# Optimization experiments

Measured on AMD Instinct MI355X. Metric: run time of the kernel, lower is better.

The kernel has to match this reference:

```python
import jax, jax.numpy as jnp
import numpy as np

DIM, D_STATE, D_CONV, EXPAND = 1024, 16, 4, 2
D_INNER = EXPAND * DIM
DT_RANK = (DIM + 15) // 16  # 64
B, L = 2, 1024


def setup_inputs() -> dict:
    key = jax.random.key(0)
    ks = jax.random.split(key, 12)
    s = lambda k, shp, sc: jax.random.normal(k, shp, jnp.float32) * sc
    return {
        "x": s(ks[0], (B, L, DIM), 1.0),
        "ln_g": jnp.ones((DIM,), jnp.float32),
        "ln_b": jnp.zeros((DIM,), jnp.float32),
        "W_in": s(ks[1], (DIM, 2 * D_INNER), DIM ** -0.5),
        "conv_w": s(ks[2], (D_INNER, D_CONV), D_CONV ** -0.5),
        "conv_b": jnp.zeros((D_INNER,), jnp.float32),
        "W_x": s(ks[3], (D_INNER, DT_RANK + 2 * D_STATE), D_INNER ** -0.5),
        "W_dt": s(ks[4], (DT_RANK, D_INNER), DT_RANK ** -0.5),
        "b_dt": s(ks[5], (D_INNER,), 0.1),
        "A_log": jnp.log(jnp.broadcast_to(jnp.arange(1, D_STATE + 1, dtype=jnp.float32), (D_INNER, D_STATE))),
        "D_skip": jnp.ones((D_INNER,), jnp.float32),
        "W_out": s(ks[6], (D_INNER, DIM), D_INNER ** -0.5),
    }


def _mamba_block(x, ln_g, ln_b, W_in, conv_w, conv_b, W_x, W_dt, b_dt, A_log, D_skip, W_out):
    # LayerNorm over feature dim
    mu = jnp.mean(x, -1, keepdims=True)
    var = jnp.mean(jnp.square(x - mu), -1, keepdims=True)
    xn = (x - mu) * jax.lax.rsqrt(var + 1e-5) * ln_g + ln_b

    # in_proj -> (u, z), each (B, L, E)
    u, z = jnp.split(xn @ W_in, 2, axis=-1)

    # causal depthwise conv1d over L (kernel D_CONV) + SiLU
    up = jnp.pad(u, ((0, 0), (D_CONV - 1, 0), (0, 0)))
    uc = conv_b
    for k in range(D_CONV):
        uc = uc + conv_w[:, k] * up[:, k:k + L, :]
    uc = jax.nn.silu(uc)

    # input-dependent dt, B, C
    dbl = uc @ W_x
    dt = jax.nn.softplus(dbl[..., :DT_RANK] @ W_dt + b_dt)      # (B,L,E)
    Bc = dbl[..., DT_RANK:DT_RANK + D_STATE]                    # (B,L,N)
    Cc = dbl[..., DT_RANK + D_STATE:]                           # (B,L,N)

    A = -jnp.exp(A_log)                                         # (E,N)
    dA = jnp.exp(dt[..., None] * A)                             # (B,L,E,N)
    dBu = (dt * uc)[..., None] * Bc[:, :, None, :]              # (B,L,E,N)

    # selective scan: h_t = dA_t * h_{t-1} + dBu_t  (associative)
    def comb(c1, c2):
        a1, b1 = c1
        a2, b2 = c2
        return a2 * a1, a2 * b1 + b2

    _, h = jax.lax.associative_scan(comb, (dA, dBu), axis=1)

    y = jnp.einsum('blen,bln->ble', h, Cc) + uc * D_skip
    y = y * jax.nn.silu(z)
    return y @ W_out                                            # (B,L,DIM)


def reference(x, ln_g, ln_b, W_in, conv_w, conv_b, W_x, W_dt, b_dt, A_log, D_skip, W_out):
    return _mamba_block(x, ln_g, ln_b, W_in, conv_w, conv_b, W_x, W_dt, b_dt, A_log, D_skip, W_out)
```

## Files before the change

### kernel.cpp

```cpp
#include <hip/hip_runtime.h>
#include <hip/hip_bf16.h>

typedef __attribute__((ext_vector_type(4))) float  f32x4;
typedef __attribute__((ext_vector_type(8))) __bf16 bf16x8;

typedef __attribute__((address_space(1))) void gvoid_t;
typedef __attribute__((address_space(3))) void lvoid_t;

__device__ __forceinline__ void gld16(const void* g, void* l) {
    __builtin_amdgcn_global_load_lds((const gvoid_t*)g, (lvoid_t*)l, 16, 0, 0);
}

template <int N> __device__ __forceinline__ void vwait() {
    if constexpr (N == 0)      asm volatile("s_waitcnt vmcnt(0)" ::: "memory");
    else if constexpr (N == 6) asm volatile("s_waitcnt vmcnt(6)" ::: "memory");
    else if constexpr (N == 8) asm volatile("s_waitcnt vmcnt(8)" ::: "memory");
}

__device__ __forceinline__ unsigned short f2bf(float f) {
    unsigned u = __builtin_bit_cast(unsigned, f);
    u += 0x7fffu + ((u >> 16) & 1u);
    return (unsigned short)(u >> 16);
}
__device__ __forceinline__ float bf2f(unsigned short u) {
    return __builtin_bit_cast(float, (unsigned)u << 16);
}
__device__ __forceinline__ float silu(float x) {
    return x / (1.f + __expf(-x));
}

__device__ __forceinline__ void tr_cvt(const float* __restrict__ in,
                                       unsigned short* __restrict__ out,
                                       int K, int N, int Npad, int bnb, int bkb,
                                       float* sh) {
    float (*t)[33] = (float(*)[33])sh;
    int bn = bnb * 32, bk = bkb * 32;
    int c = threadIdx.x & 31, r0 = threadIdx.x >> 5;
    #pragma unroll
    for (int rr = r0; rr < 32; rr += 8) {
        int k = bk + rr, n = bn + c;
        t[rr][c] = (k < K && n < N) ? in[(size_t)k * N + n] : 0.f;
    }
    __syncthreads();
    #pragma unroll
    for (int rr = r0; rr < 32; rr += 8) {
        int n = bn + rr, k = bk + c;
        if (n < Npad && k < K) out[(size_t)n * K + k] = f2bf(t[c][rr]);
    }
}

__global__ __launch_bounds__(256) void k_prep(const float* __restrict__ x,
                                              const float* __restrict__ g,
                                              const float* __restrict__ b,
                                              unsigned short* __restrict__ xn,
                                              const float* __restrict__ W_in,  unsigned short* __restrict__ WIN_T,
                                              const float* __restrict__ W_out, unsigned short* __restrict__ WOUT_T,
                                              const float* __restrict__ W_dt,  unsigned short* __restrict__ WDT_T,
                                              const float* __restrict__ W_x,   unsigned short* __restrict__ WX_T) {
    __shared__ float sh[32 * 33];
    int bid = blockIdx.x;
    if (bid < 2048) {
        int row = bid;
        const float4* xr = (const float4*)(x + (size_t)row * 1024);
        float4 v = xr[threadIdx.x];
        float s  = v.x + v.y + v.z + v.w;
        float ss = v.x*v.x + v.y*v.y + v.z*v.z + v.w*v.w;
        #pragma unroll
        for (int o = 32; o > 0; o >>= 1) { s += __shfl_down(s, o); ss += __shfl_down(ss, o); }
        if ((threadIdx.x & 63) == 0) { sh[threadIdx.x >> 6] = s; sh[4 + (threadIdx.x >> 6)] = ss; }
        __syncthreads();
        s  = sh[0] + sh[1] + sh[2] + sh[3];
        ss = sh[4] + sh[5] + sh[6] + sh[7];
        float mu  = s * (1.f / 1024.f);
        float inv = rsqrtf(ss * (1.f / 1024.f) - mu * mu + 1e-5f);
        float4 gv = ((const float4*)g)[threadIdx.x];
        float4 bv = ((const float4*)b)[threadIdx.x];
        ushort4 o4;
        o4.x = f2bf((v.x - mu) * inv * gv.x + bv.x);
        o4.y = f2bf((v.y - mu) * inv * gv.y + bv.y);
        o4.z = f2bf((v.z - mu) * inv * gv.z + bv.z);
        o4.w = f2bf((v.w - mu) * inv * gv.w + bv.w);
        ((ushort4*)xn)[(size_t)row * 256 + threadIdx.x] = o4;
    } else if (bid < 6144) {
        int i = bid - 2048;  tr_cvt(W_in,  WIN_T,  1024, 4096, 4096, i & 127, i >> 7, sh);
    } else if (bid < 8192) {
        int i = bid - 6144;  tr_cvt(W_out, WOUT_T, 2048, 1024, 1024, i & 31,  i >> 5, sh);
    } else if (bid < 8320) {
        int i = bid - 8192;  tr_cvt(W_dt,  WDT_T,  64,   2048, 2048, i & 63,  i >> 6, sh);
    } else {
        int i = bid - 8320;  tr_cvt(W_x,   WX_T,   2048, 96,   128,  i & 3,   i >> 2, sh);
    }
}

template <int BM, int BN, int EPI>
__global__ __launch_bounds__(256) void k_gemm2(const unsigned short* __restrict__ A,
                                               const unsigned short* __restrict__ Bt,
                                               float* __restrict__ C,
                                               unsigned short* __restrict__ C2,
                                               unsigned short* __restrict__ C3,
                                               int kchunk, int lda, int ldb, int ldc,
                                               size_t zstride,
                                               const float* __restrict__ bias) {
    constexpr int PA = BM / 32, PB = BN / 32, NV = PA + PB;
    constexpr int MF = BM / 32, NF = BN / 32;
    __shared__ __attribute__((aligned(16))) unsigned short smA[2 * BM * 64];
    __shared__ __attribute__((aligned(16))) unsigned short smB[2 * BN * 64];

    int tid = threadIdx.x, wave = tid >> 6, lane = tid & 63;
    int bm = blockIdx.x * BM, bn = blockIdx.y * BN;
    int kstart = blockIdx.z * kchunk;
    int nt = kchunk >> 6;
    C += (size_t)blockIdx.z * zstride;
    int wm = (wave >> 1) * (BM / 2), wn = (wave & 1) * (BN / 2);
    int lr = lane & 15, lq = lane >> 4;
    int srow = wave * 8 + (lane >> 3);
    int scg  = lane & 7;

    f32x4 acc[MF][NF] = {};

    auto STAGE = [&](int buf, int k0) {
        unsigned short* dA = smA + buf * (BM * 64) + wave * 512;
        unsigned short* dB = smB + buf * (BN * 64) + wave * 512;
        #pragma unroll
        for (int p = 0; p < PA; ++p) {
            int row = p * 32 + srow;
            int gcol = ((scg ^ (row & 7)) << 3) + k0;
            gld16(A + (size_t)(bm + row) * lda + gcol, dA + p * 2048);
        }
        #pragma unroll
        for (int p = 0; p < PB; ++p) {
            int row = p * 32 + srow;
            int gcol = ((scg ^ (row & 7)) << 3) + k0;
            gld16(Bt + (size_t)(bn + row) * ldb + gcol, dB + p * 2048);
        }
    };

    STAGE(0, kstart);
    for (int t = 0; t < nt; ++t) {
        int cur = t & 1;
        if (t + 1 < nt) { STAGE(cur ^ 1, kstart + (t + 1) * 64); vwait<NV>(); }
        else            { vwait<0>(); }
        __builtin_amdgcn_s_barrier();
        const unsigned short* sA = smA + cur * (BM * 64);
        const unsigned short* sB = smB + cur * (BN * 64);
        #pragma unroll
        for (int ks = 0; ks < 2; ++ks) {
            int cg = (ks * 4 + lq) ^ (lr & 7);
            bf16x8 af[MF], bfv[NF];
            #pragma unroll
            for (int i = 0; i < MF; ++i)
                af[i] = *(const bf16x8*)(sA + (wm + i * 16 + lr) * 64 + (cg << 3));
            #pragma unroll
            for (int i = 0; i < NF; ++i)
                bfv[i] = *(const bf16x8*)(sB + (wn + i * 16 + lr) * 64 + (cg << 3));
            #pragma unroll
            for (int mi = 0; mi < MF; ++mi)
                #pragma unroll
                for (int ni = 0; ni < NF; ++ni)
                    acc[mi][ni] = __builtin_amdgcn_mfma_f32_16x16x32_bf16(af[mi], bfv[ni], acc[mi][ni], 0, 0, 0);
        }
        __builtin_amdgcn_s_barrier();
    }

    #pragma unroll
    for (int mi = 0; mi < MF; ++mi) {
        #pragma unroll
        for (int ni = 0; ni < NF; ++ni) {
            int c = bn + wn + ni * 16 + lr;
            #pragma unroll
            for (int v = 0; v < 4; ++v) {
                int r = bm + wm + mi * 16 + (lq << 2) + v;
                float val = acc[mi][ni][v];
                if (EPI == 0) {
                    C[(size_t)r * ldc + c] = val;
                } else if (EPI == 1) {
                    val += bias[c];
                    val = (val > 20.f) ? val : log1pf(__expf(val));
                    C[(size_t)r * ldc + c] = val;
                } else {
                    if (c < 2048) C2[(size_t)r * 2048 + c] = f2bf(val);
                    else          C3[(size_t)r * 2048 + (c - 2048)] = f2bf(silu(val));
                }
            }
        }
    }
}

__global__ __launch_bounds__(256) void k_red8(const float* __restrict__ part,
                                              float* __restrict__ dbl,
                                              unsigned short* __restrict__ dtr) {
    int idx = blockIdx.x * 256 + threadIdx.x;
    float s = 0.f;
    #pragma unroll
    for (int z = 0; z < 8; ++z) s += part[(size_t)z * 262144 + idx];
    dbl[idx] = s;
    int r = idx >> 7, c = idx & 127;
    if (c < 64) dtr[r * 64 + c] = f2bf(s);
}

__global__ __launch_bounds__(256) void k_conv2(const unsigned short* __restrict__ UB,
                                               const float* __restrict__ cw,
                                               const float* __restrict__ cb,
                                               unsigned short* __restrict__ ucb) {
    int idx = blockIdx.x * 256 + threadIdx.x;
    int e  = idx & 2047;
    int bl = idx >> 11;
    int l  = bl & 1023;
    float acc = cb[e];
    float4 wv = *(const float4*)(cw + e * 4);
    float w4[4] = {wv.x, wv.y, wv.z, wv.w};
    #pragma unroll
    for (int k = 0; k < 4; ++k) {
        int ls = l - 3 + k;
        if (ls >= 0) acc += w4[k] * bf2f(UB[(size_t)(bl - 3 + k) * 2048 + e]);
    }
    ucb[idx] = f2bf(silu(acc));
}


__global__ __launch_bounds__(256) void k_scan_p1(const unsigned short* __restrict__ ucb,
                                                 const float* __restrict__ dt,
                                                 const float* __restrict__ dbl,
                                                 const float* __restrict__ A_log,
                                                 float* __restrict__ aggH,
                                                 float* __restrict__ sdtb) {
    __shared__ float sB[32][16];
    int bid = blockIdx.x;
    int c = bid & 31, eblk = (bid >> 5) & 7, b = bid >> 8;
    int t = threadIdx.x;
    int e = eblk * 256 + t;
    int bl0 = b * 1024 + c * 32;
    if (t < 128) {
        int r = t >> 2, j4 = t & 3;
        *(float4*)&sB[r][j4 * 4] = *(const float4*)(dbl + (size_t)(bl0 + r) * 128 + 64 + j4 * 4);
    }
    __syncthreads();
    float Aen[16];
    #pragma unroll
    for (int n = 0; n < 16; ++n) Aen[n] = -__expf(A_log[e * 16 + n]);
    bool fastA = true;
    #pragma unroll
    for (int n = 1; n < 16; ++n)
        fastA = fastA && (fabsf(Aen[n] - (n + 1) * Aen[0]) <= 1e-3f);
    float h[16];
    #pragma unroll
    for (int n = 0; n < 16; ++n) h[n] = 0.f;
    float sdt = 0.f;
    size_t iu = (size_t)bl0 * 2048 + e;
    #pragma unroll 4
    for (int l = 0; l < 32; ++l) {
        float dtv = dt[iu];
        float ucv = bf2f(ucb[iu]);
        float dtu = dtv * ucv;
        float dA[16];
        if (fastA) {
            float p = __expf(dtv * Aen[0]);
            float cur = p;
            #pragma unroll
            for (int n = 0; n < 16; ++n) { dA[n] = cur; cur *= p; }
        } else {
            #pragma unroll
            for (int n = 0; n < 16; ++n) dA[n] = __expf(dtv * Aen[n]);
        }
        #pragma unroll
        for (int n = 0; n < 16; ++n)
            h[n] = fmaf(dA[n], h[n], dtu * sB[l][n]);
        sdt += dtv;
        iu += 2048;
    }
    size_t o = ((size_t)(b * 32 + c) * 16) * 2048 + e;
    #pragma unroll
    for (int n = 0; n < 16; ++n) aggH[o + (size_t)n * 2048] = h[n];
    sdtb[(size_t)(b * 32 + c) * 2048 + e] = sdt;
}

__global__ __launch_bounds__(256) void k_scan_p3(const unsigned short* __restrict__ ucb,
                                                 const float* __restrict__ dt,
                                                 const float* __restrict__ dbl,
                                                 const unsigned short* __restrict__ sz,
                                                 const float* __restrict__ A_log,
                                                 const float* __restrict__ D_skip,
                                                 const float* __restrict__ aggH,
                                                 const float* __restrict__ sdtb,
                                                 unsigned short* __restrict__ yg) {
    __shared__ float sBC[32][32];
    int bid = blockIdx.x;
    int c = bid & 31, eblk = (bid >> 5) & 7, b = bid >> 8;
    int t = threadIdx.x;
    int e = eblk * 256 + t;
    int bl0 = b * 1024 + c * 32;
    {
        int r = t >> 3, j = t & 7;
        *(float4*)&sBC[r][j * 4] = *(const float4*)(dbl + (size_t)(bl0 + r) * 128 + 64 + j * 4);
    }
    __syncthreads();
    float Aen[16];
    #pragma unroll
    for (int n = 0; n < 16; ++n) Aen[n] = -__expf(A_log[e * 16 + n]);
    bool fastA = true;
    #pragma unroll
    for (int n = 1; n < 16; ++n)
        fastA = fastA && (fabsf(Aen[n] - (n + 1) * Aen[0]) <= 1e-3f);
    float De = D_skip[e];
    float h[16];
    #pragma unroll
    for (int n = 0; n < 16; ++n) h[n] = 0.f;
    for (int cc = 0; cc < c; ++cc) {
        float sdtc = sdtb[(size_t)(b * 32 + cc) * 2048 + e];
        size_t oa = ((size_t)(b * 32 + cc) * 16) * 2048 + e;
        float aa[16];
        if (fastA) {
            float p = __expf(sdtc * Aen[0]);
            float cur = p;
            #pragma unroll
            for (int n = 0; n < 16; ++n) { aa[n] = cur; cur *= p; }
        } else {
            #pragma unroll
            for (int n = 0; n < 16; ++n) aa[n] = __expf(sdtc * Aen[n]);
        }
        #pragma unroll
        for (int n = 0; n < 16; ++n)
            h[n] = fmaf(aa[n], h[n], aggH[oa + (size_t)n * 2048]);
    }
    size_t iu = (size_t)bl0 * 2048 + e;
    #pragma unroll 4
    for (int l = 0; l < 32; ++l) {
        float dtv = dt[iu];
        float ucv = bf2f(ucb[iu]);
        float szv = bf2f(sz[iu]);
        float dtu = dtv * ucv;
        float dA[16];
        if (fastA) {
            float p = __expf(dtv * Aen[0]);
            float cur = p;
            #pragma unroll
            for (int n = 0; n < 16; ++n) { dA[n] = cur; cur *= p; }
        } else {
            #pragma unroll
            for (int n = 0; n < 16; ++n) dA[n] = __expf(dtv * Aen[n]);
        }
        float y = 0.f;
        #pragma unroll
        for (int n = 0; n < 16; ++n) {
            h[n] = fmaf(dA[n], h[n], dtu * sBC[l][n]);
            y = fmaf(h[n], sBC[l][16 + n], y);
        }
        y = (y + ucv * De) * szv;
        yg[iu] = f2bf(y);
        iu += 2048;
    }
}

extern "C" void kernel_launch(void* const* d_in, const int* in_sizes, int n_in,
                              void* d_out, int out_size, void* d_ws, size_t ws_size,
                              hipStream_t stream) {
    const float* x      = (const float*)d_in[0];
    const float* ln_g   = (const float*)d_in[1];
    const float* ln_b   = (const float*)d_in[2];
    const float* W_in   = (const float*)d_in[3];
    const float* conv_w = (const float*)d_in[4];
    const float* conv_b = (const float*)d_in[5];
    const float* W_x    = (const float*)d_in[6];
    const float* W_dt   = (const float*)d_in[7];
    const float* b_dt   = (const float*)d_in[8];
    const float* A_log  = (const float*)d_in[9];
    const float* D_skip = (const float*)d_in[10];
    const float* W_out  = (const float*)d_in[11];
    float* out = (float*)d_out;

    const size_t needed =
        (size_t)4096 * 1024 * 2 + (size_t)1024 * 2048 * 2 + (size_t)2048 * 64 * 2 +
        (size_t)128 * 2048 * 2 + (size_t)2048 * 1024 * 2 + (size_t)2048 * 4096 * 4 +
        (size_t)2048 * 2048 * 4 + (size_t)2048 * 2048 * 2 + (size_t)2048 * 128 * 4 +
        (size_t)2048 * 64 * 2 + (size_t)2048 * 2048 * 4 + (size_t)2048 * 2048 * 2;
    if (ws_size < needed) return;

    char* w = (char*)d_ws;
    unsigned short* WIN_T  = (unsigned short*)w; w += (size_t)4096 * 1024 * 2;
    unsigned short* WOUT_T = (unsigned short*)w; w += (size_t)1024 * 2048 * 2;
    unsigned short* WDT_T  = (unsigned short*)w; w += (size_t)2048 * 64 * 2;
    unsigned short* WX_T   = (unsigned short*)w; w += (size_t)128 * 2048 * 2;
    unsigned short* XN     = (unsigned short*)w; w += (size_t)2048 * 1024 * 2;
    unsigned short* UB     = (unsigned short*)w; w += (size_t)2048 * 2048 * 2;
    unsigned short* SZ     = (unsigned short*)w; w += (size_t)2048 * 2048 * 2;
    unsigned short* UCB    = (unsigned short*)w; w += (size_t)2048 * 2048 * 2;
    float*          DBL    = (float*)w;          w += (size_t)2048 * 128 * 4;
    unsigned short* DTR    = (unsigned short*)w; w += (size_t)2048 * 64 * 2;
    float*          DT     = (float*)w;          w += (size_t)2048 * 2048 * 4;
    unsigned short* YG     = (unsigned short*)w; w += (size_t)2048 * 2048 * 2;

    float* PART = (float*)WIN_T;
    float* AGGH = (float*)WIN_T;
    float* SDT  = (float*)XN;

    k_prep<<<8576, 256, 0, stream>>>(x, ln_g, ln_b, XN,
                                     W_in, WIN_T, W_out, WOUT_T, W_dt, WDT_T, W_x, WX_T);

    k_gemm2<128, 128, 2><<<dim3(16, 32, 1), 256, 0, stream>>>(XN, WIN_T, nullptr, UB, SZ, 1024, 1024, 1024, 2048, 0, nullptr);

    k_conv2<<<16384, 256, 0, stream>>>(UB, conv_w, conv_b, UCB);

    k_gemm2<64, 128, 0><<<dim3(32, 1, 8), 256, 0, stream>>>(UCB, WX_T, PART, nullptr, nullptr, 256, 2048, 2048, 128, (size_t)2048 * 128, nullptr);

    k_red8<<<1024, 256, 0, stream>>>(PART, DBL, DTR);

    k_gemm2<128, 128, 1><<<dim3(16, 16, 1), 256, 0, stream>>>(DTR, WDT_T, DT, nullptr, nullptr, 64, 64, 64, 2048, 0, b_dt);

    k_scan_p1<<<512, 256, 0, stream>>>(UCB, DT, DBL, A_log, AGGH, SDT);
    k_scan_p3<<<512, 256, 0, stream>>>(UCB, DT, DBL, SZ, A_log, D_skip, AGGH, SDT, YG);

    k_gemm2<64, 128, 0><<<dim3(32, 8, 1), 256, 0, stream>>>(YG, WOUT_T, out, nullptr, nullptr, 2048, 2048, 2048, 1024, 0, nullptr);
}
```

Baseline: 273.8 us.

## Add chunk-carry scan pass and shorten dA power dependency chain

Adds a separate k_scan_p2 kernel that runs the sequential carry across the 32 chunks once per (b, n, e) and writes an initial state per chunk. k_scan_p3 then loads that state directly instead of having each chunk replay all previous chunk aggregates, which was quadratic work with a load imbalance across chunks. The dA powers are now built by repeated squaring to shorten the serial multiply chain, and the y reduction is split into four accumulators to add instruction-level parallelism. The cost is one extra kernel launch and an extra write and read of the initial-state buffer, which reuses the UB workspace.

Result: faster. 250.0 us (-8.7%).

```diff
diff --git a/kernel.cpp b/kernel.cpp
--- a/kernel.cpp
+++ b/kernel.cpp
@@ -27,6 +27,25 @@
 }
 __device__ __forceinline__ float silu(float x) {
     return x / (1.f + __expf(-x));
+}
+
+__device__ __forceinline__ void powers16(float p, float* dA) {
+    float p2 = p * p, p4 = p2 * p2, p8 = p4 * p4, p16 = p8 * p8;
+    float q[5] = {p, p2, p4, p8, p16};
+    #pragma unroll
+    for (int n = 0; n < 16; ++n) {
+        int m = n + 1;
+        float r = 1.f;
+        bool first = true;
+        #pragma unroll
+        for (int bit = 0; bit < 5; ++bit) {
+            if (m & (1 << bit)) {
+                r = first ? q[bit] : r * q[bit];
+                first = false;
+            }
+        }
+        dA[n] = r;
+    }
 }
 
 __device__ __forceinline__ void tr_cvt(const float* __restrict__ in,
@@ -254,10 +273,7 @@
         float dtu = dtv * ucv;
         float dA[16];
         if (fastA) {
-            float p = __expf(dtv * Aen[0]);
-            float cur = p;
-            #pragma unroll
-            for (int n = 0; n < 16; ++n) { dA[n] = cur; cur *= p; }
+            powers16(__expf(dtv * Aen[0]), dA);
         } else {
             #pragma unroll
             for (int n = 0; n < 16; ++n) dA[n] = __expf(dtv * Aen[n]);
@@ -272,6 +288,25 @@
     #pragma unroll
     for (int n = 0; n < 16; ++n) aggH[o + (size_t)n * 2048] = h[n];
     sdtb[(size_t)(b * 32 + c) * 2048 + e] = sdt;
+}
+
+__global__ __launch_bounds__(256) void k_scan_p2(const float* __restrict__ aggH,
+                                                 const float* __restrict__ sdtb,
+                                                 const float* __restrict__ A_log,
+                                                 float* __restrict__ hinit) {
+    int idx = blockIdx.x * 256 + threadIdx.x;
+    int b = idx >> 15;
+    int n = (idx >> 11) & 15;
+    int e = idx & 2047;
+    float Aen = -__expf(A_log[e * 16 + n]);
+    float h = 0.f;
+    #pragma unroll 4
+    for (int c = 0; c < 32; ++c) {
+        size_t base = ((size_t)(b * 32 + c) * 16 + n) * 2048 + e;
+        hinit[base] = h;
+        float a = __expf(sdtb[(size_t)(b * 32 + c) * 2048 + e] * Aen);
+        h = fmaf(a, h, aggH[base]);
+    }
 }
 
 __global__ __launch_bounds__(256) void k_scan_p3(const unsigned short* __restrict__ ucb,
@@ -280,8 +315,7 @@
                                                  const unsigned short* __restrict__ sz,
                                                  const float* __restrict__ A_log,
                                                  const float* __restrict__ D_skip,
-                                                 const float* __restrict__ aggH,
-                                                 const float* __restrict__ sdtb,
+                                                 const float* __restrict__ hinit,
                                                  unsigned short* __restrict__ yg) {
     __shared__ float sBC[32][32];
     int bid = blockIdx.x;
@@ -302,26 +336,10 @@
     for (int n = 1; n < 16; ++n)
         fastA = fastA && (fabsf(Aen[n] - (n + 1) * Aen[0]) <= 1e-3f);
     float De = D_skip[e];
+    size_t o = ((size_t)(b * 32 + c) * 16) * 2048 + e;
     float h[16];
     #pragma unroll
-    for (int n = 0; n < 16; ++n) h[n] = 0.f;
-    for (int cc = 0; cc < c; ++cc) {
-        float sdtc = sdtb[(size_t)(b * 32 + cc) * 2048 + e];
-        size_t oa = ((size_t)(b * 32 + cc) * 16) * 2048 + e;
-        float aa[16];
-        if (fastA) {
-            float p = __expf(sdtc * Aen[0]);
-            float cur = p;
-            #pragma unroll
-            for (int n = 0; n < 16; ++n) { aa[n] = cur; cur *= p; }
-        } else {
-            #pragma unroll
-            for (int n = 0; n < 16; ++n) aa[n] = __expf(sdtc * Aen[n]);
-        }
-        #pragma unroll
-        for (int n = 0; n < 16; ++n)
-            h[n] = fmaf(aa[n], h[n], aggH[oa + (size_t)n * 2048]);
-    }
+    for (int n = 0; n < 16; ++n) h[n] = hinit[o + (size_t)n * 2048];
     size_t iu = (size_t)bl0 * 2048 + e;
     #pragma unroll 4
     for (int l = 0; l < 32; ++l) {
@@ -331,20 +349,24 @@
         float dtu = dtv * ucv;
         float dA[16];
         if (fastA) {
-            float p = __expf(dtv * Aen[0]);
-            float cur = p;
-            #pragma unroll
-            for (int n = 0; n < 16; ++n) { dA[n] = cur; cur *= p; }
+            powers16(__expf(dtv * Aen[0]), dA);
         } else {
             #pragma unroll
             for (int n = 0; n < 16; ++n) dA[n] = __expf(dtv * Aen[n]);
         }
-        float y = 0.f;
-        #pragma unroll
-        for (int n = 0; n < 16; ++n) {
-            h[n] = fmaf(dA[n], h[n], dtu * sBC[l][n]);
-            y = fmaf(h[n], sBC[l][16 + n], y);
-        }
+        float y0 = 0.f, y1 = 0.f, y2 = 0.f, y3 = 0.f;
+        #pragma unroll
+        for (int n = 0; n < 16; n += 4) {
+            h[n]     = fmaf(dA[n],     h[n],     dtu * sBC[l][n]);
+            h[n + 1] = fmaf(dA[n + 1], h[n + 1], dtu * sBC[l][n + 1]);
+            h[n + 2] = fmaf(dA[n + 2], h[n + 2], dtu * sBC[l][n + 2]);
+            h[n + 3] = fmaf(dA[n + 3], h[n + 3], dtu * sBC[l][n + 3]);
+            y0 = fmaf(h[n],     sBC[l][16 + n],     y0);
+            y1 = fmaf(h[n + 1], sBC[l][16 + n + 1], y1);
+            y2 = fmaf(h[n + 2], sBC[l][16 + n + 2], y2);
+            y3 = fmaf(h[n + 3], sBC[l][16 + n + 3], y3);
+        }
+        float y = (y0 + y1) + (y2 + y3);
         y = (y + ucv * De) * szv;
         yg[iu] = f2bf(y);
         iu += 2048;
@@ -389,9 +411,10 @@
     float*          DT     = (float*)w;          w += (size_t)2048 * 2048 * 4;
     unsigned short* YG     = (unsigned short*)w; w += (size_t)2048 * 2048 * 2;
 
-    float* PART = (float*)WIN_T;
-    float* AGGH = (float*)WIN_T;
-    float* SDT  = (float*)XN;
+    float* PART  = (float*)WIN_T;
+    float* AGGH  = (float*)WIN_T;
+    float* SDT   = (float*)XN;
+    float* HINIT = (float*)UB;
 
     k_prep<<<8576, 256, 0, stream>>>(x, ln_g, ln_b, XN,
                                      W_in, WIN_T, W_out, WOUT_T, W_dt, WDT_T, W_x, WX_T);
@@ -407,7 +430,8 @@
     k_gemm2<128, 128, 1><<<dim3(16, 16, 1), 256, 0, stream>>>(DTR, WDT_T, DT, nullptr, nullptr, 64, 64, 64, 2048, 0, b_dt);
 
     k_scan_p1<<<512, 256, 0, stream>>>(UCB, DT, DBL, A_log, AGGH, SDT);
-    k_scan_p3<<<512, 256, 0, stream>>>(UCB, DT, DBL, SZ, A_log, D_skip, AGGH, SDT, YG);
+    k_scan_p2<<<256, 256, 0, stream>>>(AGGH, SDT, A_log, HINIT);
+    k_scan_p3<<<512, 256, 0, stream>>>(UCB, DT, DBL, SZ, A_log, D_skip, HINIT, YG);
 
     k_gemm2<64, 128, 0><<<dim3(32, 8, 1), 256, 0, stream>>>(YG, WOUT_T, out, nullptr, nullptr, 2048, 2048, 2048, 1024, 0, nullptr);
 }
```
